# Optimization experiments

Hardware: AMD Instinct MI355X
Metric: run time of the kernel (lower is better)

The kernel has to match this reference:

```python
import jax, jax.numpy as jnp
import numpy as np

EPS = 1e-15
PROJ_EPS = 1e-05


def project_hyp_vec(x):
    # clamp squared norm from below at 1 - PROJ_EPS (torch.clamp with min only)
    norm = jnp.sum(x * x, axis=-1, keepdims=True)
    return x * (1.0 - PROJ_EPS) / jnp.maximum(norm, 1.0 - PROJ_EPS)


def atanh(x):
    return 0.5 * jnp.log((1.0 + x) / (1.0 - x))


def mob_add(u, v):
    v = v + EPS
    norm_uv = 2.0 * jnp.sum(u * v, axis=-1, keepdims=True)
    norm_u = jnp.sum(u * u, axis=-1, keepdims=True)
    norm_v = jnp.sum(v * v, axis=-1, keepdims=True)
    denom = 1.0 + norm_uv + norm_v * norm_u
    result = (1.0 + norm_uv + norm_v) / denom * u + (1.0 - norm_u) / denom * v
    return project_hyp_vec(result)


def mob_mat_mul(M, x):
    x = project_hyp_vec(x)
    Mx = x @ M                                   # [B, H]
    Mx_norm = jnp.linalg.norm(Mx + EPS, axis=-1, keepdims=True)
    x_norm = jnp.linalg.norm(x + EPS, axis=-1, keepdims=True)
    return project_hyp_vec(jnp.tanh(Mx_norm / x_norm * atanh(x_norm)) / Mx_norm * Mx)


def setup_inputs() -> dict:
    key = jax.random.key(0)
    k_in, k_w, k_u = jax.random.split(key, 3)
    B, S, I, H = 256, 512, 256, 256
    inputs = jax.random.normal(k_in, (B, S, I), dtype=jnp.float32) * 0.1
    k = (1.0 / H) ** 0.5
    w = jax.random.uniform(k_w, (H, H), minval=-k, maxval=k, dtype=jnp.float32)
    u = jax.random.uniform(k_u, (I, H), minval=-k, maxval=k, dtype=jnp.float32)
    b = jnp.zeros((H,), dtype=jnp.float32)
    return {"inputs": inputs, "w": w, "u": u, "b": b}


def reference(inputs, w, u, b):
    B, S, I = inputs.shape
    H = w.shape[0]

    def step(h, x):
        Wh = mob_mat_mul(w, h)          # [B, H]
        Ux = mob_mat_mul(u, x)          # [B, H]
        h_new = mob_add(mob_add(Wh, Ux), b)
        return h_new, h_new

    h0 = jnp.zeros((B, H), dtype=inputs.dtype)
    _, outs = jax.lax.scan(step, h0, jnp.swapaxes(inputs, 0, 1))  # [S, B, H]
    return jnp.swapaxes(outs, 0, 1)  # [B, S, H]
```

## Files before the change

### kernel.cpp

```cpp
#include <hip/hip_runtime.h>

#define EPSV 1e-15f
#define PEPS 1e-5f

__device__ __forceinline__ float frcp(float x) { return __builtin_amdgcn_rcpf(x); }
__device__ __forceinline__ float fexp2(float x) { return __builtin_amdgcn_exp2f(x); }
__device__ __forceinline__ float flog2(float x) { return __builtin_amdgcn_logf(x); }
__device__ __forceinline__ float projscale(float n2) {
  return n2 > (1.f - PEPS) ? (1.f - PEPS) * frcp(n2) : 1.f;
}

__global__ __launch_bounds__(256) void ux_kernel(
    const float* __restrict__ x, const float* __restrict__ u,
    float* __restrict__ out)
{
  __shared__ __align__(16) float xsT[256][36];

  const int tid = threadIdx.x;
  const int lane = tid & 63, wv = tid >> 6;
  const long long base = (long long)blockIdx.x * 32;

  #pragma unroll
  for (int k4 = 0; k4 < 8; ++k4) {
    float t0 = x[(base + k4 * 4 + 0) * 256 + tid];
    float t1 = x[(base + k4 * 4 + 1) * 256 + tid];
    float t2 = x[(base + k4 * 4 + 2) * 256 + tid];
    float t3 = x[(base + k4 * 4 + 3) * 256 + tid];
    float4 v; v.x = t0; v.y = t1; v.z = t2; v.w = t3;
    *reinterpret_cast<float4*>(&xsT[tid][k4 * 4]) = v;
  }
  __syncthreads();

  float s1[8], s2[8];
  #pragma unroll
  for (int r = 0; r < 8; ++r) { s1[r] = 0.f; s2[r] = 0.f; }
  #pragma unroll
  for (int c = 0; c < 4; ++c) {
    const int i = lane + 64 * c;
    float4 xa = *reinterpret_cast<const float4*>(&xsT[i][8 * wv]);
    float4 xb = *reinterpret_cast<const float4*>(&xsT[i][8 * wv + 4]);
    s1[0] += xa.x; s2[0] += xa.x * xa.x;
    s1[1] += xa.y; s2[1] += xa.y * xa.y;
    s1[2] += xa.z; s2[2] += xa.z * xa.z;
    s1[3] += xa.w; s2[3] += xa.w * xa.w;
    s1[4] += xb.x; s2[4] += xb.x * xb.x;
    s1[5] += xb.y; s2[5] += xb.y * xb.y;
    s1[6] += xb.z; s2[6] += xb.z * xb.z;
    s1[7] += xb.w; s2[7] += xb.w * xb.w;
  }
  #pragma unroll
  for (int off = 32; off; off >>= 1) {
    #pragma unroll
    for (int r = 0; r < 8; ++r) {
      s1[r] += __shfl_xor(s1[r], off);
      s2[r] += __shfl_xor(s2[r], off);
    }
  }
  float rs[8], xnr[8];
  #pragma unroll
  for (int r = 0; r < 8; ++r) {
    float sc = projscale(s2[r]);
    rs[r] = sc;
    xnr[r] = sqrtf(sc * sc * s2[r] + 2.f * sc * EPSV * s1[r] + 256.f * EPSV * EPSV);
  }

  float4 acc[8];
  #pragma unroll
  for (int r = 0; r < 8; ++r) { acc[r].x = 0.f; acc[r].y = 0.f; acc[r].z = 0.f; acc[r].w = 0.f; }
  #pragma unroll 2
  for (int i = 0; i < 256; ++i) {
    float4 uv = *reinterpret_cast<const float4*>(&u[i * 256 + 4 * lane]);
    float4 xa = *reinterpret_cast<const float4*>(&xsT[i][8 * wv]);
    float4 xb = *reinterpret_cast<const float4*>(&xsT[i][8 * wv + 4]);
    acc[0].x += uv.x * xa.x; acc[0].y += uv.y * xa.x; acc[0].z += uv.z * xa.x; acc[0].w += uv.w * xa.x;
    acc[1].x += uv.x * xa.y; acc[1].y += uv.y * xa.y; acc[1].z += uv.z * xa.y; acc[1].w += uv.w * xa.y;
    acc[2].x += uv.x * xa.z; acc[2].y += uv.y * xa.z; acc[2].z += uv.z * xa.z; acc[2].w += uv.w * xa.z;
    acc[3].x += uv.x * xa.w; acc[3].y += uv.y * xa.w; acc[3].z += uv.z * xa.w; acc[3].w += uv.w * xa.w;
    acc[4].x += uv.x * xb.x; acc[4].y += uv.y * xb.x; acc[4].z += uv.z * xb.x; acc[4].w += uv.w * xb.x;
    acc[5].x += uv.x * xb.y; acc[5].y += uv.y * xb.y; acc[5].z += uv.z * xb.y; acc[5].w += uv.w * xb.y;
    acc[6].x += uv.x * xb.z; acc[6].y += uv.y * xb.z; acc[6].z += uv.z * xb.z; acc[6].w += uv.w * xb.z;
    acc[7].x += uv.x * xb.w; acc[7].y += uv.y * xb.w; acc[7].z += uv.z * xb.w; acc[7].w += uv.w * xb.w;
  }

  float t1s[8], t2s[8];
  #pragma unroll
  for (int r = 0; r < 8; ++r) {
    t1s[r] = acc[r].x + acc[r].y + acc[r].z + acc[r].w;
    t2s[r] = acc[r].x * acc[r].x + acc[r].y * acc[r].y + acc[r].z * acc[r].z + acc[r].w * acc[r].w;
  }
  #pragma unroll
  for (int off = 32; off; off >>= 1) {
    #pragma unroll
    for (int r = 0; r < 8; ++r) {
      t1s[r] += __shfl_xor(t1s[r], off);
      t2s[r] += __shfl_xor(t2s[r], off);
    }
  }
  #pragma unroll
  for (int r = 0; r < 8; ++r) {
    float Sm  = rs[r] * t1s[r];
    float Sm2 = rs[r] * rs[r] * t2s[r];
    float mxn = sqrtf(Sm2 + 2.f * EPSV * Sm + 256.f * EPSV * EPSV);
    float xn = xnr[r];
    float at = 0.34657359f * flog2((1.f + xn) * frcp(1.f - xn));
    float arg = mxn * frcp(xn) * at;
    float e2 = fexp2(arg * 2.8853902f);
    float th = 1.f - 2.f * frcp(e2 + 1.f);
    float g = th * frcp(mxn);
    float fs = g * projscale(g * g * Sm2) * rs[r];
    float4 o;
    o.x = fs * acc[r].x; o.y = fs * acc[r].y; o.z = fs * acc[r].z; o.w = fs * acc[r].w;
    reinterpret_cast<float4*>(out)[(base + 8 * wv + r) * 64 + lane] = o;
  }
}

__global__ __launch_bounds__(512, 2) void rnn_kernel(
    const float* __restrict__ w, const float* __restrict__ bvec,
    float* __restrict__ out, int S)
{
  __shared__ __align__(16) float h_lds[256];
  __shared__ __align__(16) float partial[8][256];
  __shared__ __align__(16) float v_lds[2][256];

  const int tid = threadIdx.x;
  const int lane = tid & 63;
  const int wv = tid >> 6;

  float4 wreg[32];
  #pragma unroll
  for (int ii = 0; ii < 32; ++ii)
    wreg[ii] = *reinterpret_cast<const float4*>(&w[(wv * 32 + ii) * 256 + 4 * lane]);

  float4 vb4 = *reinterpret_cast<const float4*>(&bvec[4 * lane]);
  vb4.x += EPSV; vb4.y += EPSV; vb4.z += EPSV; vb4.w += EPSV;

  float S_vb  = vb4.x + vb4.y + vb4.z + vb4.w;
  float S_vb2 = vb4.x * vb4.x + vb4.y * vb4.y + vb4.z * vb4.z + vb4.w * vb4.w;
  #pragma unroll
  for (int off = 32; off; off >>= 1) {
    S_vb  += __shfl_xor(S_vb, off);
    S_vb2 += __shfl_xor(S_vb2, off);
  }

  const long long rb4 = (long long)blockIdx.x * S * 64;
  const float4* outv = reinterpret_cast<const float4*>(out);
  float4* outw = reinterpret_cast<float4*>(out);

  float4 vnext;
  if (wv == 0) {
    reinterpret_cast<float4*>(h_lds)[lane] = float4{0.f, 0.f, 0.f, 0.f};
    reinterpret_cast<float4*>(v_lds[0])[lane] = outv[rb4 + lane];
    vnext = outv[rb4 + 64 + lane];
  }
  __syncthreads();

  float S_h = 0.f, S_h2 = 0.f;

  for (int t = 0; t < S; ++t) {
    float4 a = {0.f, 0.f, 0.f, 0.f};
    const float4* hp = reinterpret_cast<const float4*>(&h_lds[wv * 32]);
    #pragma unroll
    for (int i4 = 0; i4 < 8; ++i4) {
      float4 h4 = hp[i4];
      float4 w0 = wreg[i4 * 4 + 0], w1 = wreg[i4 * 4 + 1];
      float4 w2 = wreg[i4 * 4 + 2], w3 = wreg[i4 * 4 + 3];
      a.x += w0.x * h4.x; a.y += w0.y * h4.x; a.z += w0.z * h4.x; a.w += w0.w * h4.x;
      a.x += w1.x * h4.y; a.y += w1.y * h4.y; a.z += w1.z * h4.y; a.w += w1.w * h4.y;
      a.x += w2.x * h4.z; a.y += w2.y * h4.z; a.z += w2.z * h4.z; a.w += w2.w * h4.z;
      a.x += w3.x * h4.w; a.y += w3.y * h4.w; a.z += w3.z * h4.w; a.w += w3.w * h4.w;
    }
    *reinterpret_cast<float4*>(&partial[wv][4 * lane]) = a;

    if (wv == 0) {
      if (t + 1 < S) reinterpret_cast<float4*>(v_lds[(t + 1) & 1])[lane] = vnext;
      if (t + 2 < S) vnext = outv[rb4 + (t + 2) * 64 + lane];
    }
    __syncthreads();

    if (wv == 0) {
      float4 m4 = {0.f, 0.f, 0.f, 0.f};
      #pragma unroll
      for (int k = 0; k < 8; ++k) {
        float4 p = *reinterpret_cast<const float4*>(&partial[k][4 * lane]);
        m4.x += p.x; m4.y += p.y; m4.z += p.z; m4.w += p.w;
      }
      float4 v4 = reinterpret_cast<const float4*>(v_lds[t & 1])[lane];
      v4.x += EPSV; v4.y += EPSV; v4.z += EPSV; v4.w += EPSV;

      float p0 = m4.x + m4.y + m4.z + m4.w;
      float p1 = m4.x * m4.x + m4.y * m4.y + m4.z * m4.z + m4.w * m4.w;
      float p2 = m4.x * v4.x + m4.y * v4.y + m4.z * v4.z + m4.w * v4.w;
      float p3 = v4.x + v4.y + v4.z + v4.w;
      float p4 = v4.x * v4.x + v4.y * v4.y + v4.z * v4.z + v4.w * v4.w;
      float p5 = m4.x * vb4.x + m4.y * vb4.y + m4.z * vb4.z + m4.w * vb4.w;
      float p6 = v4.x * vb4.x + v4.y * vb4.y + v4.z * vb4.z + v4.w * vb4.w;
      #pragma unroll
      for (int off = 32; off; off >>= 1) {
        p0 += __shfl_xor(p0, off); p1 += __shfl_xor(p1, off);
        p2 += __shfl_xor(p2, off); p3 += __shfl_xor(p3, off);
        p4 += __shfl_xor(p4, off); p5 += __shfl_xor(p5, off);
        p6 += __shfl_xor(p6, off);
      }
      const float S_Mx = p0, S_Mx2 = p1, S_Mxv = p2, S_v = p3, S_v2 = p4,
                  S_Mxb = p5, S_vvb = p6;

      float s_hp = projscale(S_h2);
      float xn = sqrtf(s_hp * s_hp * S_h2 + 2.f * s_hp * EPSV * S_h + 256.f * EPSV * EPSV);
      float mxn = sqrtf(S_Mx2 + 2.f * EPSV * S_Mx + 256.f * EPSV * EPSV);
      float at = 0.34657359f * flog2((1.f + xn) * frcp(1.f - xn));
      float arg = mxn * frcp(xn) * at;
      float e2 = fexp2(arg * 2.8853902f);
      float th = 1.f - 2.f * frcp(e2 + 1.f);
      float g = th * frcp(mxn);
      float beta = g * projscale(g * g * S_Mx2);

      float nuv = 2.f * beta * S_Mxv;
      float nu  = beta * beta * S_Mx2;
      float nv  = S_v2;
      float rden = frcp(1.f + nuv + nv * nu);
      float cA = (1.f + nuv + nv) * rden;
      float cB = (1.f - nu) * rden;
      float cAb = cA * beta;
      float S_r1  = cAb * S_Mx + cB * S_v;
      float S_r12 = cAb * cAb * S_Mx2 + 2.f * cAb * cB * S_Mxv + cB * cB * S_v2;
      float S_r1b = cAb * S_Mxb + cB * S_vvb;
      float s1p = projscale(S_r12);
      float S_U = s1p * S_r1, S_U2 = s1p * s1p * S_r12, S_Ub = s1p * S_r1b;

      float nuv2 = 2.f * S_Ub;
      float rden2 = frcp(1.f + nuv2 + S_vb2 * S_U2);
      float dA = (1.f + nuv2 + S_vb2) * rden2;
      float dB = (1.f - S_U2) * rden2;
      float S_hn  = dA * S_U + dB * S_vb;
      float S_hn2 = dA * dA * S_U2 + 2.f * dA * dB * S_Ub + dB * dB * S_vb2;
      float s2p = projscale(S_hn2);

      float km = s2p * dA * s1p * cAb;
      float kv = s2p * dA * s1p * cB;
      float kb = s2p * dB;

      float4 hn;
      hn.x = km * m4.x + kv * v4.x + kb * vb4.x;
      hn.y = km * m4.y + kv * v4.y + kb * vb4.y;
      hn.z = km * m4.z + kv * v4.z + kb * vb4.z;
      hn.w = km * m4.w + kv * v4.w + kb * vb4.w;
      outw[rb4 + t * 64 + lane] = hn;

      S_h  = s2p * S_hn;
      S_h2 = s2p * s2p * S_hn2;
      float snext = projscale(S_h2);
      float4 hq;
      hq.x = snext * hn.x; hq.y = snext * hn.y; hq.z = snext * hn.z; hq.w = snext * hn.w;
      reinterpret_cast<float4*>(h_lds)[lane] = hq;
    }
    __syncthreads();
  }
}

extern "C" void kernel_launch(void* const* d_in, const int* in_sizes, int n_in,
                              void* d_out, int out_size, void* d_ws, size_t ws_size,
                              hipStream_t stream) {
  const float* x = (const float*)d_in[0];
  const float* w = (const float*)d_in[1];
  const float* u = (const float*)d_in[2];
  const float* b = (const float*)d_in[3];
  float* out = (float*)d_out;

  const int nrows = in_sizes[0] / 256;
  const int S = 512;
  const int B = nrows / S;

  ux_kernel<<<nrows / 32, 256, 0, stream>>>(x, u, out);
  rnn_kernel<<<B, 512, 0, stream>>>(w, b, out, S);
}
```

Baseline: 961.3 us.

## Use linearity of W to overlap recurrent matvec with Ux term via warp specialization

The recurrent kernel now gives one wave to the scalar/elementwise update and eight waves to matvec work. Since h_new is a linear combination of Mx, Ux and b, the eight waves compute W·Mx and W·Ux in the same pass, reading the Ux vector directly from LDS. The control wave then assembles the next Mx from these partials plus precomputed W·b and W·1 terms, instead of forming h and then multiplying. This restructures the per-step dependency chain and the barrier schedule. In exchange it doubles the FMA work per step, changes rounding behaviour, and drops occupancy to one 576-thread block per CU.

```diff
diff --git a/kernel.cpp b/kernel.cpp
--- a/kernel.cpp
+++ b/kernel.cpp
@@ -114,77 +114,112 @@
   }
 }
 
-__global__ __launch_bounds__(512, 2) void rnn_kernel(
+__global__ __launch_bounds__(576, 1) void rnn_kernel(
     const float* __restrict__ w, const float* __restrict__ bvec,
     float* __restrict__ out, int S)
 {
-  __shared__ __align__(16) float h_lds[256];
-  __shared__ __align__(16) float partial[8][256];
+  __shared__ __align__(16) float mx_lds[256];
   __shared__ __align__(16) float v_lds[2][256];
+  __shared__ __align__(16) float pP[8][256];
+  __shared__ __align__(16) float pQ[8][256];
 
   const int tid = threadIdx.x;
   const int lane = tid & 63;
   const int wv = tid >> 6;
 
-  float4 wreg[32];
-  #pragma unroll
-  for (int ii = 0; ii < 32; ++ii)
-    wreg[ii] = *reinterpret_cast<const float4*>(&w[(wv * 32 + ii) * 256 + 4 * lane]);
-
-  float4 vb4 = *reinterpret_cast<const float4*>(&bvec[4 * lane]);
-  vb4.x += EPSV; vb4.y += EPSV; vb4.z += EPSV; vb4.w += EPSV;
-
-  float S_vb  = vb4.x + vb4.y + vb4.z + vb4.w;
-  float S_vb2 = vb4.x * vb4.x + vb4.y * vb4.y + vb4.z * vb4.z + vb4.w * vb4.w;
-  #pragma unroll
-  for (int off = 32; off; off >>= 1) {
-    S_vb  += __shfl_xor(S_vb, off);
-    S_vb2 += __shfl_xor(S_vb2, off);
-  }
-
   const long long rb4 = (long long)blockIdx.x * S * 64;
   const float4* outv = reinterpret_cast<const float4*>(out);
   float4* outw = reinterpret_cast<float4*>(out);
 
-  float4 vnext;
-  if (wv == 0) {
-    reinterpret_cast<float4*>(h_lds)[lane] = float4{0.f, 0.f, 0.f, 0.f};
-    reinterpret_cast<float4*>(v_lds[0])[lane] = outv[rb4 + lane];
-    vnext = outv[rb4 + 64 + lane];
-  }
-  __syncthreads();
-
-  float S_h = 0.f, S_h2 = 0.f;
-
-  for (int t = 0; t < S; ++t) {
-    float4 a = {0.f, 0.f, 0.f, 0.f};
-    const float4* hp = reinterpret_cast<const float4*>(&h_lds[wv * 32]);
-    #pragma unroll
-    for (int i4 = 0; i4 < 8; ++i4) {
-      float4 h4 = hp[i4];
-      float4 w0 = wreg[i4 * 4 + 0], w1 = wreg[i4 * 4 + 1];
-      float4 w2 = wreg[i4 * 4 + 2], w3 = wreg[i4 * 4 + 3];
-      a.x += w0.x * h4.x; a.y += w0.y * h4.x; a.z += w0.z * h4.x; a.w += w0.w * h4.x;
-      a.x += w1.x * h4.y; a.y += w1.y * h4.y; a.z += w1.z * h4.y; a.w += w1.w * h4.y;
-      a.x += w2.x * h4.z; a.y += w2.y * h4.z; a.z += w2.z * h4.z; a.w += w2.w * h4.z;
-      a.x += w3.x * h4.w; a.y += w3.y * h4.w; a.z += w3.z * h4.w; a.w += w3.w * h4.w;
-    }
-    *reinterpret_cast<float4*>(&partial[wv][4 * lane]) = a;
-
-    if (wv == 0) {
-      if (t + 1 < S) reinterpret_cast<float4*>(v_lds[(t + 1) & 1])[lane] = vnext;
-      if (t + 2 < S) vnext = outv[rb4 + (t + 2) * 64 + lane];
-    }
-    __syncthreads();
-
-    if (wv == 0) {
-      float4 m4 = {0.f, 0.f, 0.f, 0.f};
+  if (wv >= 1) {
+    const int ks = (wv - 1) * 32;
+    float4 wreg[32];
+    #pragma unroll
+    for (int ii = 0; ii < 32; ++ii)
+      wreg[ii] = *reinterpret_cast<const float4*>(&w[(ks + ii) * 256 + 4 * lane]);
+
+    __syncthreads();
+    {
+      float4 p = {0.f,0.f,0.f,0.f}, q = {0.f,0.f,0.f,0.f};
+      const float4* vbp = reinterpret_cast<const float4*>(&v_lds[0][ks]);
       #pragma unroll
-      for (int k = 0; k < 8; ++k) {
-        float4 p = *reinterpret_cast<const float4*>(&partial[k][4 * lane]);
-        m4.x += p.x; m4.y += p.y; m4.z += p.z; m4.w += p.w;
+      for (int i4 = 0; i4 < 8; ++i4) {
+        float4 b4 = vbp[i4];
+        float4 w0 = wreg[i4*4+0], w1 = wreg[i4*4+1], w2 = wreg[i4*4+2], w3 = wreg[i4*4+3];
+        p.x += w0.x*b4.x; p.y += w0.y*b4.x; p.z += w0.z*b4.x; p.w += w0.w*b4.x;
+        p.x += w1.x*b4.y; p.y += w1.y*b4.y; p.z += w1.z*b4.y; p.w += w1.w*b4.y;
+        p.x += w2.x*b4.z; p.y += w2.y*b4.z; p.z += w2.z*b4.z; p.w += w2.w*b4.z;
+        p.x += w3.x*b4.w; p.y += w3.y*b4.w; p.z += w3.z*b4.w; p.w += w3.w*b4.w;
+        q.x += (w0.x + w1.x) + (w2.x + w3.x);
+        q.y += (w0.y + w1.y) + (w2.y + w3.y);
+        q.z += (w0.z + w1.z) + (w2.z + w3.z);
+        q.w += (w0.w + w1.w) + (w2.w + w3.w);
       }
-      float4 v4 = reinterpret_cast<const float4*>(v_lds[t & 1])[lane];
+      *reinterpret_cast<float4*>(&pP[wv-1][4*lane]) = p;
+      *reinterpret_cast<float4*>(&pQ[wv-1][4*lane]) = q;
+    }
+    __syncthreads();
+    __syncthreads();
+
+    for (int t = 0; t < S; ++t) {
+      float4 p = {0.f,0.f,0.f,0.f}, q = {0.f,0.f,0.f,0.f};
+      const float4* hp = reinterpret_cast<const float4*>(&mx_lds[ks]);
+      const float4* vp = reinterpret_cast<const float4*>(&v_lds[t & 1][ks]);
+      #pragma unroll
+      for (int i4 = 0; i4 < 8; ++i4) {
+        float4 h4 = hp[i4];
+        float4 v4 = vp[i4];
+        float4 w0 = wreg[i4*4+0], w1 = wreg[i4*4+1], w2 = wreg[i4*4+2], w3 = wreg[i4*4+3];
+        p.x += w0.x*h4.x; p.y += w0.y*h4.x; p.z += w0.z*h4.x; p.w += w0.w*h4.x;
+        p.x += w1.x*h4.y; p.y += w1.y*h4.y; p.z += w1.z*h4.y; p.w += w1.w*h4.y;
+        p.x += w2.x*h4.z; p.y += w2.y*h4.z; p.z += w2.z*h4.z; p.w += w2.w*h4.z;
+        p.x += w3.x*h4.w; p.y += w3.y*h4.w; p.z += w3.z*h4.w; p.w += w3.w*h4.w;
+        q.x += w0.x*v4.x; q.y += w0.y*v4.x; q.z += w0.z*v4.x; q.w += w0.w*v4.x;
+        q.x += w1.x*v4.y; q.y += w1.y*v4.y; q.z += w1.z*v4.y; q.w += w1.w*v4.y;
+        q.x += w2.x*v4.z; q.y += w2.y*v4.z; q.z += w2.z*v4.z; q.w += w2.w*v4.z;
+        q.x += w3.x*v4.w; q.y += w3.y*v4.w; q.z += w3.z*v4.w; q.w += w3.w*v4.w;
+      }
+      *reinterpret_cast<float4*>(&pP[wv-1][4*lane]) = p;
+      *reinterpret_cast<float4*>(&pQ[wv-1][4*lane]) = q;
+      __syncthreads();
+      __syncthreads();
+    }
+  } else {
+    float4 vb4 = *reinterpret_cast<const float4*>(&bvec[4 * lane]);
+    vb4.x += EPSV; vb4.y += EPSV; vb4.z += EPSV; vb4.w += EPSV;
+
+    float S_vb  = vb4.x + vb4.y + vb4.z + vb4.w;
+    float S_vb2 = vb4.x * vb4.x + vb4.y * vb4.y + vb4.z * vb4.z + vb4.w * vb4.w;
+    #pragma unroll
+    for (int off = 32; off; off >>= 1) {
+      S_vb  += __shfl_xor(S_vb, off);
+      S_vb2 += __shfl_xor(S_vb2, off);
+    }
+
+    reinterpret_cast<float4*>(mx_lds)[lane] = float4{0.f,0.f,0.f,0.f};
+    reinterpret_cast<float4*>(v_lds[0])[lane] = vb4;
+    __syncthreads();
+
+    float4 vA = outv[rb4 + lane];
+    float4 vB = outv[rb4 + 64 + lane];
+    __syncthreads();
+
+    float4 Wvb4 = {0.f,0.f,0.f,0.f}, W1_4 = {0.f,0.f,0.f,0.f};
+    #pragma unroll
+    for (int k = 0; k < 8; ++k) {
+      float4 pp = *reinterpret_cast<const float4*>(&pP[k][4*lane]);
+      float4 qq = *reinterpret_cast<const float4*>(&pQ[k][4*lane]);
+      Wvb4.x += pp.x; Wvb4.y += pp.y; Wvb4.z += pp.z; Wvb4.w += pp.w;
+      W1_4.x += qq.x; W1_4.y += qq.y; W1_4.z += qq.z; W1_4.w += qq.w;
+    }
+    reinterpret_cast<float4*>(v_lds[0])[lane] = vA;
+    __syncthreads();
+
+    float4 m4 = {0.f,0.f,0.f,0.f};
+    float S_h = 0.f, S_h2 = 0.f;
+
+    for (int t = 0; t < S; ++t) {
+      float4 v4 = vA;
       v4.x += EPSV; v4.y += EPSV; v4.z += EPSV; v4.w += EPSV;
 
       float p0 = m4.x + m4.y + m4.z + m4.w;
@@ -249,11 +284,30 @@
       S_h  = s2p * S_hn;
       S_h2 = s2p * s2p * S_hn2;
       float snext = projscale(S_h2);
-      float4 hq;
-      hq.x = snext * hn.x; hq.y = snext * hn.y; hq.z = snext * hn.z; hq.w = snext * hn.w;
-      reinterpret_cast<float4*>(h_lds)[lane] = hq;
-    }
-    __syncthreads();
+
+      if (t + 1 < S) reinterpret_cast<float4*>(v_lds[(t + 1) & 1])[lane] = vB;
+      float4 vC = vB;
+      if (t + 2 < S) vC = outv[rb4 + (t + 2) * 64 + lane];
+
+      __syncthreads();
+
+      float4 Pc = {0.f,0.f,0.f,0.f}, Qc = {0.f,0.f,0.f,0.f};
+      #pragma unroll
+      for (int k = 0; k < 8; ++k) {
+        float4 pp = *reinterpret_cast<const float4*>(&pP[k][4*lane]);
+        float4 qq = *reinterpret_cast<const float4*>(&pQ[k][4*lane]);
+        Pc.x += pp.x; Pc.y += pp.y; Pc.z += pp.z; Pc.w += pp.w;
+        Qc.x += qq.x; Qc.y += qq.y; Qc.z += qq.z; Qc.w += qq.w;
+      }
+      m4.x = snext * (km * Pc.x + kv * (Qc.x + EPSV * W1_4.x) + kb * Wvb4.x);
+      m4.y = snext * (km * Pc.y + kv * (Qc.y + EPSV * W1_4.y) + kb * Wvb4.y);
+      m4.z = snext * (km * Pc.z + kv * (Qc.z + EPSV * W1_4.z) + kb * Wvb4.z);
+      m4.w = snext * (km * Pc.w + kv * (Qc.w + EPSV * W1_4.w) + kb * Wvb4.w);
+      reinterpret_cast<float4*>(mx_lds)[lane] = m4;
+
+      vA = vB; vB = vC;
+      __syncthreads();
+    }
   }
 }
 
@@ -271,5 +325,5 @@
   const int B = nrows / S;
 
   ux_kernel<<<nrows / 32, 256, 0, stream>>>(x, u, out);
-  rnn_kernel<<<B, 512, 0, stream>>>(w, b, out, S);
+  rnn_kernel<<<B, 576, 0, stream>>>(w, b, out, S);
 }
```

After: 899.9 us. 1.07x faster.

## Restructure recurrence via linearity of W, DPP reductions, precomputed input stats

Applied to the files above, without the earlier changes.

The recurrence is rewritten using linearity: next step's Mx is formed as km*W·m + kv*W·v + kb*W·b, so the matvec on step t's inputs can start before h is known and the scalar chain runs on wave 0 with fewer barriers. W is split unevenly (wave 0 holds 4 rows, the others 36 each), and partial sums are accumulated with LDS atomics into double-buffered psum/qsum. Wave reductions switch from shuffles to DPP plus readlane, and ux_kernel writes per-row v statistics to the workspace so the recurrence skips those reductions. The cost is more register pressure, LDS atomics on the critical path, and a dependence on workspace size.

```diff
diff --git a/kernel.cpp b/kernel.cpp
--- a/kernel.cpp
+++ b/kernel.cpp
@@ -2,6 +2,8 @@
 
 #define EPSV 1e-15f
 #define PEPS 1e-5f
+
+typedef float v2f __attribute__((ext_vector_type(2)));
 
 __device__ __forceinline__ float frcp(float x) { return __builtin_amdgcn_rcpf(x); }
 __device__ __forceinline__ float fexp2(float x) { return __builtin_amdgcn_exp2f(x); }
@@ -10,9 +12,32 @@
   return n2 > (1.f - PEPS) ? (1.f - PEPS) * frcp(n2) : 1.f;
 }
 
+template <int CTRL>
+__device__ __forceinline__ float dppadd(float x) {
+  int y = __builtin_amdgcn_update_dpp(0, __float_as_int(x), CTRL, 0xF, 0xF, true);
+  return x + __int_as_float(y);
+}
+__device__ __forceinline__ float wave_sum(float x) {
+  x = dppadd<0x111>(x);
+  x = dppadd<0x112>(x);
+  x = dppadd<0x114>(x);
+  x = dppadd<0x118>(x);
+  x = dppadd<0x142>(x);
+  x = dppadd<0x143>(x);
+  return __int_as_float(__builtin_amdgcn_readlane(__float_as_int(x), 63));
+}
+
+__device__ __forceinline__ float4 ld4s(const float* p, int lane) {
+  return float4{p[lane], p[lane + 64], p[lane + 128], p[lane + 192]};
+}
+__device__ __forceinline__ void st4s(float* p, int lane, float4 v) {
+  p[lane] = v.x; p[lane + 64] = v.y; p[lane + 128] = v.z; p[lane + 192] = v.w;
+}
+
 __global__ __launch_bounds__(256) void ux_kernel(
     const float* __restrict__ x, const float* __restrict__ u,
-    float* __restrict__ out)
+    const float* __restrict__ bvec, float* __restrict__ out,
+    float4* __restrict__ vstat, int use_vstat)
 {
   __shared__ __align__(16) float xsT[256][36];
 
@@ -30,6 +55,10 @@
     *reinterpret_cast<float4*>(&xsT[tid][k4 * 4]) = v;
   }
   __syncthreads();
+
+  float4 bb = *reinterpret_cast<const float4*>(&bvec[4 * lane]);
+  bb.x += EPSV; bb.y += EPSV; bb.z += EPSV; bb.w += EPSV;
+  float S_vbrow = wave_sum(bb.x + bb.y + bb.z + bb.w);
 
   float s1[8], s2[8];
   #pragma unroll
@@ -48,20 +77,14 @@
     s1[6] += xb.z; s2[6] += xb.z * xb.z;
     s1[7] += xb.w; s2[7] += xb.w * xb.w;
   }
-  #pragma unroll
-  for (int off = 32; off; off >>= 1) {
-    #pragma unroll
-    for (int r = 0; r < 8; ++r) {
-      s1[r] += __shfl_xor(s1[r], off);
-      s2[r] += __shfl_xor(s2[r], off);
-    }
-  }
   float rs[8], xnr[8];
   #pragma unroll
   for (int r = 0; r < 8; ++r) {
-    float sc = projscale(s2[r]);
+    float a = wave_sum(s1[r]);
+    float b2 = wave_sum(s2[r]);
+    float sc = projscale(b2);
     rs[r] = sc;
-    xnr[r] = sqrtf(sc * sc * s2[r] + 2.f * sc * EPSV * s1[r] + 256.f * EPSV * EPSV);
+    xnr[r] = sqrtf(sc * sc * b2 + 2.f * sc * EPSV * a + 256.f * EPSV * EPSV);
   }
 
   float4 acc[8];
@@ -82,24 +105,14 @@
     acc[7].x += uv.x * xb.w; acc[7].y += uv.y * xb.w; acc[7].z += uv.z * xb.w; acc[7].w += uv.w * xb.w;
   }
 
-  float t1s[8], t2s[8];
   #pragma unroll
   for (int r = 0; r < 8; ++r) {
-    t1s[r] = acc[r].x + acc[r].y + acc[r].z + acc[r].w;
-    t2s[r] = acc[r].x * acc[r].x + acc[r].y * acc[r].y + acc[r].z * acc[r].z + acc[r].w * acc[r].w;
-  }
-  #pragma unroll
-  for (int off = 32; off; off >>= 1) {
-    #pragma unroll
-    for (int r = 0; r < 8; ++r) {
-      t1s[r] += __shfl_xor(t1s[r], off);
-      t2s[r] += __shfl_xor(t2s[r], off);
-    }
-  }
-  #pragma unroll
-  for (int r = 0; r < 8; ++r) {
-    float Sm  = rs[r] * t1s[r];
-    float Sm2 = rs[r] * rs[r] * t2s[r];
+    float t1 = wave_sum(acc[r].x + acc[r].y + acc[r].z + acc[r].w);
+    float t2 = wave_sum(acc[r].x * acc[r].x + acc[r].y * acc[r].y +
+                        acc[r].z * acc[r].z + acc[r].w * acc[r].w);
+    float t3 = wave_sum(acc[r].x * bb.x + acc[r].y * bb.y + acc[r].z * bb.z + acc[r].w * bb.w);
+    float Sm  = rs[r] * t1;
+    float Sm2 = rs[r] * rs[r] * t2;
     float mxn = sqrtf(Sm2 + 2.f * EPSV * Sm + 256.f * EPSV * EPSV);
     float xn = xnr[r];
     float at = 0.34657359f * flog2((1.f + xn) * frcp(1.f - xn));
@@ -109,100 +122,125 @@
     float g = th * frcp(mxn);
     float fs = g * projscale(g * g * Sm2) * rs[r];
     float4 o;
-    o.x = fs * acc[r].x; o.y = fs * acc[r].y; o.z = fs * acc[r].z; o.w = fs * acc[r].w;
+    o.x = fs * acc[r].x + EPSV; o.y = fs * acc[r].y + EPSV;
+    o.z = fs * acc[r].z + EPSV; o.w = fs * acc[r].w + EPSV;
     reinterpret_cast<float4*>(out)[(base + 8 * wv + r) * 64 + lane] = o;
-  }
-}
+    if (use_vstat && lane == 0) {
+      float Sv  = fs * t1 + 256.f * EPSV;
+      float Sv2 = fs * fs * t2 + 2.f * EPSV * fs * t1 + 256.f * EPSV * EPSV;
+      float Svb = fs * t3 + EPSV * S_vbrow;
+      vstat[base + 8 * wv + r] = float4{Sv, Sv2, Svb, 0.f};
+    }
+  }
+}
+
+template <int NR>
+__device__ __forceinline__ void load_w(const float* __restrict__ w, int rb, int lane, v2f* wr) {
+  #pragma unroll
+  for (int r = 0; r < NR; ++r) {
+    const float* p = &w[(rb + r) * 256 + lane];
+    float a = p[0], b = p[64], c = p[128], d = p[192];
+    asm volatile("" : "+v"(a), "+v"(b), "+v"(c), "+v"(d));
+    wr[2 * r]     = v2f{a, b};
+    wr[2 * r + 1] = v2f{c, d};
+  }
+}
+
+template <int NR>
+__device__ __forceinline__ void mv_pq(const v2f* wr, const float* mxp, const float* vp,
+                                      float4& P, float4& Q) {
+  v2f pl{0.f, 0.f}, ph{0.f, 0.f}, ql{0.f, 0.f}, qh{0.f, 0.f};
+  #pragma unroll
+  for (int i = 0; i < NR / 4; ++i) {
+    float4 h4 = *reinterpret_cast<const float4*>(mxp + 4 * i);
+    float4 u4 = *reinterpret_cast<const float4*>(vp + 4 * i);
+    pl += wr[8 * i + 0] * h4.x; ph += wr[8 * i + 1] * h4.x;
+    pl += wr[8 * i + 2] * h4.y; ph += wr[8 * i + 3] * h4.y;
+    pl += wr[8 * i + 4] * h4.z; ph += wr[8 * i + 5] * h4.z;
+    pl += wr[8 * i + 6] * h4.w; ph += wr[8 * i + 7] * h4.w;
+    ql += wr[8 * i + 0] * u4.x; qh += wr[8 * i + 1] * u4.x;
+    ql += wr[8 * i + 2] * u4.y; qh += wr[8 * i + 3] * u4.y;
+    ql += wr[8 * i + 4] * u4.z; qh += wr[8 * i + 5] * u4.z;
+    ql += wr[8 * i + 6] * u4.w; qh += wr[8 * i + 7] * u4.w;
+  }
+  P = float4{pl.x, pl.y, ph.x, ph.y};
+  Q = float4{ql.x, ql.y, qh.x, qh.y};
+}
+
+#define ATOMIC_PQ(b)                                             \
+  atomicAdd(&psum[b][lane],       P.x);                          \
+  atomicAdd(&psum[b][lane + 64],  P.y);                          \
+  atomicAdd(&psum[b][lane + 128], P.z);                          \
+  atomicAdd(&psum[b][lane + 192], P.w);                          \
+  atomicAdd(&qsum[b][lane],       Q.x);                          \
+  atomicAdd(&qsum[b][lane + 64],  Q.y);                          \
+  atomicAdd(&qsum[b][lane + 128], Q.z);                          \
+  atomicAdd(&qsum[b][lane + 192], Q.w);
 
 __global__ __launch_bounds__(512, 2) void rnn_kernel(
     const float* __restrict__ w, const float* __restrict__ bvec,
-    float* __restrict__ out, int S)
+    float* __restrict__ out, const float4* __restrict__ vstat, int S, int use_vstat)
 {
-  __shared__ __align__(16) float h_lds[256];
-  __shared__ __align__(16) float partial[8][256];
+  __shared__ __align__(16) float mx_lds[256];
   __shared__ __align__(16) float v_lds[2][256];
+  __shared__ __align__(16) float psum[2][256];
+  __shared__ __align__(16) float qsum[2][256];
 
   const int tid = threadIdx.x;
   const int lane = tid & 63;
   const int wv = tid >> 6;
 
-  float4 wreg[32];
-  #pragma unroll
-  for (int ii = 0; ii < 32; ++ii)
-    wreg[ii] = *reinterpret_cast<const float4*>(&w[(wv * 32 + ii) * 256 + 4 * lane]);
-
-  float4 vb4 = *reinterpret_cast<const float4*>(&bvec[4 * lane]);
-  vb4.x += EPSV; vb4.y += EPSV; vb4.z += EPSV; vb4.w += EPSV;
-
-  float S_vb  = vb4.x + vb4.y + vb4.z + vb4.w;
-  float S_vb2 = vb4.x * vb4.x + vb4.y * vb4.y + vb4.z * vb4.z + vb4.w * vb4.w;
-  #pragma unroll
-  for (int off = 32; off; off >>= 1) {
-    S_vb  += __shfl_xor(S_vb, off);
-    S_vb2 += __shfl_xor(S_vb2, off);
-  }
-
-  const long long rb4 = (long long)blockIdx.x * S * 64;
-  const float4* outv = reinterpret_cast<const float4*>(out);
-  float4* outw = reinterpret_cast<float4*>(out);
-
-  float4 vnext;
+  const long long rowbase = (long long)blockIdx.x * S * 256;
+  const long long vsbase = (long long)blockIdx.x * S;
+  const float4 zero4{0.f, 0.f, 0.f, 0.f};
+
   if (wv == 0) {
-    reinterpret_cast<float4*>(h_lds)[lane] = float4{0.f, 0.f, 0.f, 0.f};
-    reinterpret_cast<float4*>(v_lds[0])[lane] = outv[rb4 + lane];
-    vnext = outv[rb4 + 64 + lane];
-  }
-  __syncthreads();
-
-  float S_h = 0.f, S_h2 = 0.f;
-
-  for (int t = 0; t < S; ++t) {
-    float4 a = {0.f, 0.f, 0.f, 0.f};
-    const float4* hp = reinterpret_cast<const float4*>(&h_lds[wv * 32]);
-    #pragma unroll
-    for (int i4 = 0; i4 < 8; ++i4) {
-      float4 h4 = hp[i4];
-      float4 w0 = wreg[i4 * 4 + 0], w1 = wreg[i4 * 4 + 1];
-      float4 w2 = wreg[i4 * 4 + 2], w3 = wreg[i4 * 4 + 3];
-      a.x += w0.x * h4.x; a.y += w0.y * h4.x; a.z += w0.z * h4.x; a.w += w0.w * h4.x;
-      a.x += w1.x * h4.y; a.y += w1.y * h4.y; a.z += w1.z * h4.y; a.w += w1.w * h4.y;
-      a.x += w2.x * h4.z; a.y += w2.y * h4.z; a.z += w2.z * h4.z; a.w += w2.w * h4.z;
-      a.x += w3.x * h4.w; a.y += w3.y * h4.w; a.z += w3.z * h4.w; a.w += w3.w * h4.w;
-    }
-    *reinterpret_cast<float4*>(&partial[wv][4 * lane]) = a;
-
-    if (wv == 0) {
-      if (t + 1 < S) reinterpret_cast<float4*>(v_lds[(t + 1) & 1])[lane] = vnext;
-      if (t + 2 < S) vnext = outv[rb4 + (t + 2) * 64 + lane];
-    }
-    __syncthreads();
-
-    if (wv == 0) {
-      float4 m4 = {0.f, 0.f, 0.f, 0.f};
-      #pragma unroll
-      for (int k = 0; k < 8; ++k) {
-        float4 p = *reinterpret_cast<const float4*>(&partial[k][4 * lane]);
-        m4.x += p.x; m4.y += p.y; m4.z += p.z; m4.w += p.w;
+    v2f wr0[8];
+    load_w<4>(w, 0, lane, wr0);
+
+    float4 vb4{bvec[lane] + EPSV, bvec[lane + 64] + EPSV,
+               bvec[lane + 128] + EPSV, bvec[lane + 192] + EPSV};
+    float S_vb  = wave_sum(vb4.x + vb4.y + vb4.z + vb4.w);
+    float S_vb2 = wave_sum(vb4.x * vb4.x + vb4.y * vb4.y + vb4.z * vb4.z + vb4.w * vb4.w);
+
+    reinterpret_cast<float4*>(mx_lds)[lane]   = zero4;
+    reinterpret_cast<float4*>(psum[0])[lane]  = zero4;
+    reinterpret_cast<float4*>(psum[1])[lane]  = zero4;
+    reinterpret_cast<float4*>(qsum[0])[lane]  = zero4;
+    reinterpret_cast<float4*>(qsum[1])[lane]  = zero4;
+    st4s(v_lds[0], lane, vb4);
+    __syncthreads();
+
+    { float4 P, Q; mv_pq<4>(wr0, &mx_lds[0], &v_lds[0][0], P, Q); ATOMIC_PQ(0) }
+    __syncthreads();
+
+    float4 Wvb4 = ld4s(qsum[0], lane);
+    reinterpret_cast<float4*>(qsum[0])[lane] = zero4;
+    float4 vA = ld4s(out + rowbase, lane);
+    float4 vB = ld4s(out + rowbase + 256, lane);
+    float4 sA{0.f,0.f,0.f,0.f}, sB{0.f,0.f,0.f,0.f};
+    if (use_vstat) { sA = vstat[vsbase]; sB = vstat[vsbase + 1]; }
+    st4s(v_lds[0], lane, vA);
+    __syncthreads();
+
+    float4 m4 = zero4;
+    float S_h = 0.f, S_h2 = 0.f;
+
+    for (int t = 0; t < S; ++t) {
+      const int b = t & 1;
+      float4 v4 = vA;
+
+      float S_Mx  = wave_sum(m4.x + m4.y + m4.z + m4.w);
+      float S_Mx2 = wave_sum(m4.x * m4.x + m4.y * m4.y + m4.z * m4.z + m4.w * m4.w);
+      float S_Mxv = wave_sum(m4.x * v4.x + m4.y * v4.y + m4.z * v4.z + m4.w * v4.w);
+      float S_Mxb = wave_sum(m4.x * vb4.x + m4.y * vb4.y + m4.z * vb4.z + m4.w * vb4.w);
+      float S_v, S_v2, S_vvb;
+      if (use_vstat) { S_v = sA.x; S_v2 = sA.y; S_vvb = sA.z; }
+      else {
+        S_v   = wave_sum(v4.x + v4.y + v4.z + v4.w);
+        S_v2  = wave_sum(v4.x * v4.x + v4.y * v4.y + v4.z * v4.z + v4.w * v4.w);
+        S_vvb = wave_sum(v4.x * vb4.x + v4.y * vb4.y + v4.z * vb4.z + v4.w * vb4.w);
       }
-      float4 v4 = reinterpret_cast<const float4*>(v_lds[t & 1])[lane];
-      v4.x += EPSV; v4.y += EPSV; v4.z += EPSV; v4.w += EPSV;
-
-      float p0 = m4.x + m4.y + m4.z + m4.w;
-      float p1 = m4.x * m4.x + m4.y * m4.y + m4.z * m4.z + m4.w * m4.w;
-      float p2 = m4.x * v4.x + m4.y * v4.y + m4.z * v4.z + m4.w * v4.w;
-      float p3 = v4.x + v4.y + v4.z + v4.w;
-      float p4 = v4.x * v4.x + v4.y * v4.y + v4.z * v4.z + v4.w * v4.w;
-      float p5 = m4.x * vb4.x + m4.y * vb4.y + m4.z * vb4.z + m4.w * vb4.w;
-      float p6 = v4.x * vb4.x + v4.y * vb4.y + v4.z * vb4.z + v4.w * vb4.w;
-      #pragma unroll
-      for (int off = 32; off; off >>= 1) {
-        p0 += __shfl_xor(p0, off); p1 += __shfl_xor(p1, off);
-        p2 += __shfl_xor(p2, off); p3 += __shfl_xor(p3, off);
-        p4 += __shfl_xor(p4, off); p5 += __shfl_xor(p5, off);
-        p6 += __shfl_xor(p6, off);
-      }
-      const float S_Mx = p0, S_Mx2 = p1, S_Mxv = p2, S_v = p3, S_v2 = p4,
-                  S_Mxb = p5, S_vvb = p6;
 
       float s_hp = projscale(S_h2);
       float xn = sqrtf(s_hp * s_hp * S_h2 + 2.f * s_hp * EPSV * S_h + 256.f * EPSV * EPSV);
@@ -239,21 +277,56 @@
       float kv = s2p * dA * s1p * cB;
       float kb = s2p * dB;
 
-      float4 hn;
-      hn.x = km * m4.x + kv * v4.x + kb * vb4.x;
-      hn.y = km * m4.y + kv * v4.y + kb * vb4.y;
-      hn.z = km * m4.z + kv * v4.z + kb * vb4.z;
-      hn.w = km * m4.w + kv * v4.w + kb * vb4.w;
-      outw[rb4 + t * 64 + lane] = hn;
+      float4 hn{km * m4.x + kv * v4.x + kb * vb4.x,
+                km * m4.y + kv * v4.y + kb * vb4.y,
+                km * m4.z + kv * v4.z + kb * vb4.z,
+                km * m4.w + kv * v4.w + kb * vb4.w};
+      st4s(out + rowbase + (long long)t * 256, lane, hn);
 
       S_h  = s2p * S_hn;
       S_h2 = s2p * s2p * S_hn2;
-      float snext = projscale(S_h2);
-      float4 hq;
-      hq.x = snext * hn.x; hq.y = snext * hn.y; hq.z = snext * hn.z; hq.w = snext * hn.w;
-      reinterpret_cast<float4*>(h_lds)[lane] = hq;
+      float snextp = projscale(S_h2);
+
+      if (t + 1 < S) st4s(v_lds[(t + 1) & 1], lane, vB);
+      float4 vC = vB, sC = sB;
+      if (t + 2 < S) {
+        vC = ld4s(out + rowbase + (long long)(t + 2) * 256, lane);
+        if (use_vstat) sC = vstat[vsbase + t + 2];
+      }
+
+      { float4 P, Q; mv_pq<4>(wr0, &mx_lds[0], &v_lds[b][0], P, Q); ATOMIC_PQ(b) }
+      __syncthreads();
+
+      float4 Pc = ld4s(psum[b], lane);
+      float4 Qc = ld4s(qsum[b], lane);
+      m4.x = snextp * (km * Pc.x + kv * Qc.x + kb * Wvb4.x);
+      m4.y = snextp * (km * Pc.y + kv * Qc.y + kb * Wvb4.y);
+      m4.z = snextp * (km * Pc.z + kv * Qc.z + kb * Wvb4.z);
+      m4.w = snextp * (km * Pc.w + kv * Qc.w + kb * Wvb4.w);
+      st4s(mx_lds, lane, m4);
+      reinterpret_cast<float4*>(psum[b])[lane] = zero4;
+      reinterpret_cast<float4*>(qsum[b])[lane] = zero4;
+      __syncthreads();
+
+      vA = vB; vB = vC; sA = sB; sB = sC;
     }
-    __syncthreads();
+  } else {
+    const int rb = 4 + (wv - 1) * 36;
+    v2f wrk[72];
+    load_w<36>(w, rb, lane, wrk);
+    __syncthreads();
+    { float4 P, Q; mv_pq<36>(wrk, &mx_lds[rb], &v_lds[0][rb], P, Q); ATOMIC_PQ(0) }
+    __syncthreads();
+    __syncthreads();
+
+    for (int t = 0; t < S; ++t) {
+      const int b = t & 1;
+      float4 P, Q;
+      mv_pq<36>(wrk, &mx_lds[rb], &v_lds[b][rb], P, Q);
+      ATOMIC_PQ(b)
+      __syncthreads();
+      __syncthreads();
+    }
   }
 }
 
@@ -270,6 +343,9 @@
   const int S = 512;
   const int B = nrows / S;
 
-  ux_kernel<<<nrows / 32, 256, 0, stream>>>(x, u, out);
-  rnn_kernel<<<B, 512, 0, stream>>>(w, b, out, S);
-}
+  const int use_vstat = (ws_size >= (size_t)nrows * 16) ? 1 : 0;
+  float4* vstat = (float4*)d_ws;
+
+  ux_kernel<<<nrows / 32, 256, 0, stream>>>(x, u, b, out, vstat, use_vstat);
+  rnn_kernel<<<B, 512, 0, stream>>>(w, b, out, vstat, S, use_vstat);
+}
```

New measurement: 3.191 ms. +231.9%, slower.
